# Optimization experiments

Measured on AMD Instinct MI355X. Metric: run time of the kernel, lower is better.

## Reference

```python
import jax, jax.numpy as jnp
import numpy as np
from jax import lax

B, T, H = 2, 1024, 2048
NH, D = 8, 128          # heads, head_dim
P = NH * D              # projection size
K = 4                   # short conv kernel size
EPS = 1e-6
SCALE = D ** -0.5


def _causal_conv_silu(x, w):
    # x: (B,T,C); w: (C,K) depthwise causal conv followed by silu (ShortConvolution)
    C = w.shape[0]
    kern = jnp.transpose(w)[:, None, :]  # (K,1,C)
    y = lax.conv_general_dilated(x, kern, window_strides=(1,), padding=[(K - 1, 0)],
                                 dimension_numbers=('NWC', 'WIO', 'NWC'),
                                 feature_group_count=C)
    return jax.nn.silu(y)


def _l2norm(x):
    return x * jax.lax.rsqrt(jnp.sum(x * x, axis=-1, keepdims=True) + EPS)


def _forward(hidden_states, Wq, Wk, Wv, conv_q, conv_k, conv_v, A_log, dt_bias,
             Wfa, Wfb, Wb, Wga, Wgb, norm_weight, Wo):
    x = hidden_states                                # (B,T,H)
    q = _causal_conv_silu(x @ Wq.T, conv_q)          # (B,T,P)
    k = _causal_conv_silu(x @ Wk.T, conv_k)
    v = _causal_conv_silu(x @ Wv.T, conv_v)
    # fused_kda_gate: g = -exp(A_log) * softplus(f_b(f_a(x)) + dt_bias), per (h,d) channel
    gf = (x @ Wfa.T) @ Wfb.T                         # (B,T,P) low-rank gate proj
    gf = gf.reshape(B, T, NH, D) + dt_bias.reshape(NH, D)
    g = -jnp.exp(A_log)[None, None, :, None] * jax.nn.softplus(gf)  # (B,T,NH,D) log-decay <= 0
    beta = jax.nn.sigmoid(x @ Wb.T)                  # (B,T,NH)
    q = _l2norm(q.reshape(B, T, NH, D)) * SCALE      # use_qk_l2norm_in_kernel + 1/sqrt(d) scale
    k = _l2norm(k.reshape(B, T, NH, D))
    v = v.reshape(B, T, NH, D)

    # gated delta-rule recurrence (KDA): per-key-channel decay, beta-weighted delta update
    def step(S, inp):
        q_t, k_t, v_t, g_t, b_t = inp                # (B,NH,D), beta (B,NH)
        S = S * jnp.exp(g_t)[..., None]              # decay rows (key dim) of S[.,.,dk,dv]
        kv = jnp.einsum('bhk,bhkv->bhv', k_t, S)
        delta = (v_t - kv) * b_t[..., None]
        S = S + jnp.einsum('bhk,bhv->bhkv', k_t, delta)
        o_t = jnp.einsum('bhk,bhkv->bhv', q_t, S)
        return S, o_t

    tfirst = lambda a: jnp.moveaxis(a, 1, 0)         # time-major for scan
    S0 = jnp.zeros((B, NH, D, D), x.dtype)
    _, o = lax.scan(step, S0, (tfirst(q), tfirst(k), tfirst(v), tfirst(g), tfirst(beta)))
    o = jnp.moveaxis(o, 0, 1)                        # (B,T,NH,D)

    # FusedRMSNormGated(sigmoid): gate applied before RMS normalization (Mamba2 convention)
    gate = ((x @ Wga.T) @ Wgb.T).reshape(B, T, NH, D)
    og = o * jax.nn.sigmoid(gate)
    og = og * jax.lax.rsqrt(jnp.mean(og * og, axis=-1, keepdims=True) + EPS) * norm_weight
    return og.reshape(B * T, P) @ Wo.T               # (B*T, H)


def setup_inputs():
    ks = jax.random.split(jax.random.key(0), 16)
    s = 0.02
    f32 = jnp.float32
    return {
        'hidden_states': jax.random.normal(ks[0], (B, T, H), f32),
        'Wq': jax.random.normal(ks[1], (P, H), f32) * s,
        'Wk': jax.random.normal(ks[2], (P, H), f32) * s,
        'Wv': jax.random.normal(ks[3], (P, H), f32) * s,
        'conv_q': jax.random.normal(ks[4], (P, K), f32) * 0.3,
        'conv_k': jax.random.normal(ks[5], (P, K), f32) * 0.3,
        'conv_v': jax.random.normal(ks[6], (P, K), f32) * 0.3,
        'A_log': jnp.log(jax.random.uniform(ks[7], (NH,), f32, 1.0, 16.0)),
        'dt_bias': jax.random.normal(ks[8], (P,), f32) * 0.5,
        'Wfa': jax.random.normal(ks[9], (D, H), f32) * s,
        'Wfb': jax.random.normal(ks[10], (P, D), f32) * s,
        'Wb': jax.random.normal(ks[11], (NH, H), f32) * s,
        'Wga': jax.random.normal(ks[12], (D, H), f32) * s,
        'Wgb': jax.random.normal(ks[13], (P, D), f32) * s,
        'norm_weight': jnp.ones((D,), f32),
        'Wo': jax.random.normal(ks[14], (H, P), f32) * s,
    }


def reference(hidden_states, Wq, Wk, Wv, conv_q, conv_k, conv_v, A_log, dt_bias,
              Wfa, Wfb, Wb, Wga, Wgb, norm_weight, Wo):
    return _forward(hidden_states, Wq, Wk, Wv, conv_q, conv_k, conv_v, A_log, dt_bias,
                    Wfa, Wfb, Wb, Wga, Wgb, norm_weight, Wo)
```

## Files before the change

kernel.cpp:

```cpp
#include <hip/hip_runtime.h>
#include <hip/hip_bf16.h>
#include <cstddef>
#include <cstdint>

#define Bb 2
#define Tt 1024
#define Hh 2048
#define NHh 8
#define Dd 128
#define Pp (NHh * Dd)
#define Kk 4
#define EPSf 1e-6f
#define SCALEf 0.08838834764831845f
#define DVQ 16
#define CHUNK 8

typedef short bf16x8 __attribute__((ext_vector_type(8)));
typedef float f32x4 __attribute__((ext_vector_type(4)));
typedef float f32x2 __attribute__((ext_vector_type(2)));

template <int CTRL>
__device__ __forceinline__ float dpp_add(float x) {
  int yi = __builtin_amdgcn_update_dpp(0, __builtin_bit_cast(int, x), CTRL, 0xF, 0xF, true);
  return x + __builtin_bit_cast(float, yi);
}
__device__ __forceinline__ float row16_sum(float x) {
  x = dpp_add<0xB1>(x);
  x = dpp_add<0x4E>(x);
  x = dpp_add<0x124>(x);
  x = dpp_add<0x128>(x);
  return x;
}

__device__ __forceinline__ void gload_lds16(const void* g, void* l) {
  __builtin_amdgcn_global_load_lds((const __attribute__((address_space(1))) void*)g,
                                   (__attribute__((address_space(3))) void*)l, 16, 0, 0);
}

__global__ __launch_bounds__(256) void cvt_bf16(const float* __restrict__ src,
                                                __hip_bfloat16* __restrict__ dst, int n) {
  const int i = (blockIdx.x * 256 + threadIdx.x) * 8;
  if (i >= n) return;
  const float4 a = *reinterpret_cast<const float4*>(src + i);
  const float4 b = *reinterpret_cast<const float4*>(src + i + 4);
  __hip_bfloat16 t[8];
  t[0] = __float2bfloat16(a.x); t[1] = __float2bfloat16(a.y);
  t[2] = __float2bfloat16(a.z); t[3] = __float2bfloat16(a.w);
  t[4] = __float2bfloat16(b.x); t[5] = __float2bfloat16(b.y);
  t[6] = __float2bfloat16(b.z); t[7] = __float2bfloat16(b.w);
  *reinterpret_cast<uint4*>(dst + i) = *reinterpret_cast<const uint4*>(t);
}

__global__ __launch_bounds__(256) void cvt_bf16_x4(const float* __restrict__ s0,
                                                   const float* __restrict__ s1,
                                                   const float* __restrict__ s2,
                                                   const float* __restrict__ s3,
                                                   __hip_bfloat16* __restrict__ d0,
                                                   __hip_bfloat16* __restrict__ d1,
                                                   __hip_bfloat16* __restrict__ d2,
                                                   __hip_bfloat16* __restrict__ d3,
                                                   int nper) {
  const int bpa = nper / 2048;
  const int a = blockIdx.x / bpa;
  const int i = (blockIdx.x % bpa) * 2048 + threadIdx.x * 8;
  const float* src = (a == 0) ? s0 : (a == 1) ? s1 : (a == 2) ? s2 : s3;
  __hip_bfloat16* dst = (a == 0) ? d0 : (a == 1) ? d1 : (a == 2) ? d2 : d3;
  const float4 x = *reinterpret_cast<const float4*>(src + i);
  const float4 y = *reinterpret_cast<const float4*>(src + i + 4);
  __hip_bfloat16 t[8];
  t[0] = __float2bfloat16(x.x); t[1] = __float2bfloat16(x.y);
  t[2] = __float2bfloat16(x.z); t[3] = __float2bfloat16(x.w);
  t[4] = __float2bfloat16(y.x); t[5] = __float2bfloat16(y.y);
  t[6] = __float2bfloat16(y.z); t[7] = __float2bfloat16(y.w);
  *reinterpret_cast<uint4*>(dst + i) = *reinterpret_cast<const uint4*>(t);
}

__global__ __launch_bounds__(256) void cvt_split(const float* __restrict__ src,
                                                 __hip_bfloat16* __restrict__ hi,
                                                 __hip_bfloat16* __restrict__ lo, int n) {
  const int i = (blockIdx.x * 256 + threadIdx.x) * 8;
  if (i >= n) return;
  __hip_bfloat16 th[8], tl[8];
#pragma unroll
  for (int j = 0; j < 2; j++) {
    const float4 a = *reinterpret_cast<const float4*>(src + i + j * 4);
    const float f[4] = {a.x, a.y, a.z, a.w};
#pragma unroll
    for (int e = 0; e < 4; e++) {
      const __hip_bfloat16 h = __float2bfloat16(f[e]);
      th[j * 4 + e] = h;
      tl[j * 4 + e] = __float2bfloat16(f[e] - __bfloat162float(h));
    }
  }
  *reinterpret_cast<uint4*>(hi + i) = *reinterpret_cast<const uint4*>(th);
  *reinterpret_cast<uint4*>(lo + i) = *reinterpret_cast<const uint4*>(tl);
}

__global__ __launch_bounds__(256) void gemm_nn_split(const float* __restrict__ A,
                                                     const float* __restrict__ B,
                                                     __hip_bfloat16* __restrict__ Chi,
                                                     __hip_bfloat16* __restrict__ Clo,
                                                     int M, int N, int K, int mode) {
  __shared__ float As[64][33];
  __shared__ float Bs[32][65];
  const int bm = blockIdx.y * 64, bn = blockIdx.x * 64;
  const int tid = threadIdx.x;
  const int tx = tid & 15, ty = tid >> 4;
  float acc[4][4];
#pragma unroll
  for (int i = 0; i < 4; i++)
#pragma unroll
    for (int j = 0; j < 4; j++) acc[i][j] = 0.f;
  for (int k0 = 0; k0 < K; k0 += 32) {
#pragma unroll
    for (int i = 0; i < 8; i++) {
      const int idx = tid + i * 256;
      const int r = idx >> 5, c = idx & 31;
      As[r][c] = A[(size_t)(bm + r) * K + k0 + c];
    }
#pragma unroll
    for (int i = 0; i < 8; i++) {
      const int idx = tid + i * 256;
      const int r = idx >> 6, c = idx & 63;
      Bs[r][c] = B[(size_t)(k0 + r) * N + bn + c];
    }
    __syncthreads();
#pragma unroll
    for (int kk = 0; kk < 32; kk++) {
      float a[4], b[4];
#pragma unroll
      for (int i = 0; i < 4; i++) a[i] = As[ty * 4 + i][kk];
#pragma unroll
      for (int j = 0; j < 4; j++) b[j] = Bs[kk][tx * 4 + j];
#pragma unroll
      for (int i = 0; i < 4; i++)
#pragma unroll
        for (int j = 0; j < 4; j++) acc[i][j] += a[i] * b[j];
    }
    __syncthreads();
  }
#pragma unroll
  for (int i = 0; i < 4; i++) {
    const int row = bm + ty * 4 + i;
#pragma unroll
    for (int j = 0; j < 4; j++) {
      const int col = bn + tx * 4 + j;
      const float v = acc[i][j];
      const __hip_bfloat16 h = __float2bfloat16(v);
      Chi[(size_t)row * N + col] = h;
      if (mode == 0) Clo[(size_t)row * N + col] = __float2bfloat16(v - __bfloat162float(h));
    }
  }
}

__global__ __launch_bounds__(256) void gemm_bf16_lds(const __hip_bfloat16* __restrict__ A,
                                                     const __hip_bfloat16* __restrict__ B,
                                                     float* __restrict__ C,
                                                     __hip_bfloat16* __restrict__ Cbf,
                                                     int M, int N, int K, int outmode) {
  __shared__ __align__(16) __hip_bfloat16 As[128 * 64];
  __shared__ __align__(16) __hip_bfloat16 Bs[128 * 64];
  const int tid = threadIdx.x;
  const int wave = tid >> 6;
  const int lane = tid & 63;
  const int wm = (wave >> 1) * 64;
  const int wn = (wave & 1) * 64;
  const int bm = blockIdx.y * 128;
  const int bn = blockIdx.x * 128;
  const int l15 = lane & 15;
  const int l4 = lane >> 4;
  const int srow = lane >> 3;
  const int scol = (lane & 7) * 8;

  f32x4 acc[4][4];
#pragma unroll
  for (int i = 0; i < 4; i++)
#pragma unroll
    for (int j = 0; j < 4; j++) acc[i][j] = (f32x4){0.f, 0.f, 0.f, 0.f};

  for (int k0 = 0; k0 < K; k0 += 64) {
#pragma unroll
    for (int i = 0; i < 4; i++) {
      const int s = wave * 4 + i;
      const int row = s * 8 + srow;
      gload_lds16(A + (size_t)(bm + row) * K + k0 + scol, &As[s * 512]);
      gload_lds16(B + (size_t)(bn + row) * K + k0 + scol, &Bs[s * 512]);
    }
    __syncthreads();
    bf16x8 af[4][2], bfv[4][2];
#pragma unroll
    for (int kf = 0; kf < 2; kf++) {
      const int kc = kf * 32 + l4 * 8;
#pragma unroll
      for (int mf = 0; mf < 4; mf++)
        af[mf][kf] = *reinterpret_cast<const bf16x8*>(&As[(wm + mf * 16 + l15) * 64 + kc]);
#pragma unroll
      for (int nf = 0; nf < 4; nf++)
        bfv[nf][kf] = *reinterpret_cast<const bf16x8*>(&Bs[(wn + nf * 16 + l15) * 64 + kc]);
    }
#pragma unroll
    for (int kf = 0; kf < 2; kf++)
#pragma unroll
      for (int mf = 0; mf < 4; mf++)
#pragma unroll
        for (int nf = 0; nf < 4; nf++)
          acc[mf][nf] = __builtin_amdgcn_mfma_f32_16x16x32_bf16(af[mf][kf], bfv[nf][kf],
                                                                acc[mf][nf], 0, 0, 0);
    __syncthreads();
  }
#pragma unroll
  for (int mf = 0; mf < 4; mf++) {
#pragma unroll
    for (int nf = 0; nf < 4; nf++) {
      const int col = bn + wn + nf * 16 + l15;
#pragma unroll
      for (int r = 0; r < 4; r++) {
        const int row = bm + wm + mf * 16 + l4 * 4 + r;
        if (outmode == 0) C[(size_t)row * N + col] = acc[mf][nf][r];
        else Cbf[(size_t)row * N + col] = __float2bfloat16(acc[mf][nf][r]);
      }
    }
  }
}

__global__ __launch_bounds__(256) void gemm_bf16_3t_lds(const __hip_bfloat16* __restrict__ Ahi,
                                                        const __hip_bfloat16* __restrict__ Alo,
                                                        const __hip_bfloat16* __restrict__ Bhi,
                                                        const __hip_bfloat16* __restrict__ Blo,
                                                        float* __restrict__ C,
                                                        int M, int N, int K,
                                                        const float* __restrict__ dtb,
                                                        const float* __restrict__ A_log,
                                                        int gmode) {
  __shared__ __align__(16) __hip_bfloat16 Ahs[64 * 64];
  __shared__ __align__(16) __hip_bfloat16 Als[64 * 64];
  __shared__ __align__(16) __hip_bfloat16 Bhs[128 * 64];
  __shared__ __align__(16) __hip_bfloat16 Bls[128 * 64];
  const int tid = threadIdx.x;
  const int wave = tid >> 6;
  const int lane = tid & 63;
  const int wm = (wave >> 1) * 32;
  const int wn = (wave & 1) * 64;
  const int bm = blockIdx.y * 64;
  const int bn = blockIdx.x * 128;
  const int l15 = lane & 15;
  const int l4 = lane >> 4;
  const int srow = lane >> 3;
  const int scol = (lane & 7) * 8;

  f32x4 acc[2][4];
#pragma unroll
  for (int i = 0; i < 2; i++)
#pragma unroll
    for (int j = 0; j < 4; j++) acc[i][j] = (f32x4){0.f, 0.f, 0.f, 0.f};

  for (int k0 = 0; k0 < K; k0 += 64) {
#pragma unroll
    for (int i = 0; i < 12; i++) {
      const int sid = wave * 12 + i;
      if (sid < 8) {
        const int row = sid * 8 + srow;
        gload_lds16(Ahi + (size_t)(bm + row) * K + k0 + scol, &Ahs[sid * 512]);
      } else if (sid < 16) {
        const int row = (sid - 8) * 8 + srow;
        gload_lds16(Alo + (size_t)(bm + row) * K + k0 + scol, &Als[(sid - 8) * 512]);
      } else if (sid < 32) {
        const int row = (sid - 16) * 8 + srow;
        gload_lds16(Bhi + (size_t)(bn + row) * K + k0 + scol, &Bhs[(sid - 16) * 512]);
      } else {
        const int row = (sid - 32) * 8 + srow;
        gload_lds16(Blo + (size_t)(bn + row) * K + k0 + scol, &Bls[(sid - 32) * 512]);
      }
    }
    __syncthreads();
#pragma unroll
    for (int kf = 0; kf < 2; kf++) {
      const int kc = kf * 32 + l4 * 8;
      bf16x8 ah[2], al[2], bh[4], bl[4];
#pragma unroll
      for (int mf = 0; mf < 2; mf++) {
        ah[mf] = *reinterpret_cast<const bf16x8*>(&Ahs[(wm + mf * 16 + l15) * 64 + kc]);
        al[mf] = *reinterpret_cast<const bf16x8*>(&Als[(wm + mf * 16 + l15) * 64 + kc]);
      }
#pragma unroll
      for (int nf = 0; nf < 4; nf++) {
        bh[nf] = *reinterpret_cast<const bf16x8*>(&Bhs[(wn + nf * 16 + l15) * 64 + kc]);
        bl[nf] = *reinterpret_cast<const bf16x8*>(&Bls[(wn + nf * 16 + l15) * 64 + kc]);
      }
#pragma unroll
      for (int mf = 0; mf < 2; mf++)
#pragma unroll
        for (int nf = 0; nf < 4; nf++) {
          acc[mf][nf] = __builtin_amdgcn_mfma_f32_16x16x32_bf16(ah[mf], bh[nf], acc[mf][nf], 0, 0, 0);
          acc[mf][nf] = __builtin_amdgcn_mfma_f32_16x16x32_bf16(ah[mf], bl[nf], acc[mf][nf], 0, 0, 0);
          acc[mf][nf] = __builtin_amdgcn_mfma_f32_16x16x32_bf16(al[mf], bh[nf], acc[mf][nf], 0, 0, 0);
        }
    }
    __syncthreads();
  }
#pragma unroll
  for (int mf = 0; mf < 2; mf++)
#pragma unroll
    for (int nf = 0; nf < 4; nf++) {
      const int col = bn + wn + nf * 16 + l15;
#pragma unroll
      for (int r = 0; r < 4; r++) {
        const int row = bm + wm + mf * 16 + l4 * 4 + r;
        float val = acc[mf][nf][r];
        if (gmode) {
          const float xv = val + dtb[col];
          const float sp = (xv > 20.f) ? xv : log1pf(expf(xv));
          val = expf(-expf(A_log[col >> 7]) * sp);
        }
        C[(size_t)row * N + col] = val;
      }
    }
}

__global__ __launch_bounds__(256) void gemm_nt(const float* __restrict__ A,
                                               const float* __restrict__ Bm,
                                               float* __restrict__ C,
                                               int M, int N, int Kd) {
  __shared__ float As[16][64];
  __shared__ float Bs[16][64];
  const int bm = blockIdx.y * 64;
  const int bn = blockIdx.x * 64;
  const int tid = threadIdx.x;
  const int tx = tid & 15;
  const int ty = tid >> 4;
  const int lr = tid >> 2;
  const int lc = (tid & 3) << 2;
  float acc[4][4];
#pragma unroll
  for (int i = 0; i < 4; i++)
#pragma unroll
    for (int j = 0; j < 4; j++) acc[i][j] = 0.f;
  for (int k0 = 0; k0 < Kd; k0 += 16) {
    float4 a4 = make_float4(0.f, 0.f, 0.f, 0.f);
    float4 b4 = make_float4(0.f, 0.f, 0.f, 0.f);
    const int ar = bm + lr;
    if (ar < M) a4 = *reinterpret_cast<const float4*>(A + (size_t)ar * Kd + k0 + lc);
    const int br = bn + lr;
    if (br < N) b4 = *reinterpret_cast<const float4*>(Bm + (size_t)br * Kd + k0 + lc);
    As[lc + 0][lr] = a4.x; As[lc + 1][lr] = a4.y; As[lc + 2][lr] = a4.z; As[lc + 3][lr] = a4.w;
    Bs[lc + 0][lr] = b4.x; Bs[lc + 1][lr] = b4.y; Bs[lc + 2][lr] = b4.z; Bs[lc + 3][lr] = b4.w;
    __syncthreads();
#pragma unroll
    for (int kk = 0; kk < 16; kk++) {
      float4 av = *reinterpret_cast<const float4*>(&As[kk][ty << 2]);
      float4 bv = *reinterpret_cast<const float4*>(&Bs[kk][tx << 2]);
      float a[4] = {av.x, av.y, av.z, av.w};
      float b[4] = {bv.x, bv.y, bv.z, bv.w};
#pragma unroll
      for (int i = 0; i < 4; i++)
#pragma unroll
        for (int j = 0; j < 4; j++) acc[i][j] += a[i] * b[j];
    }
    __syncthreads();
  }
#pragma unroll
  for (int i = 0; i < 4; i++) {
    const int row = bm + (ty << 2) + i;
    if (row >= M) continue;
#pragma unroll
    for (int j = 0; j < 4; j++) {
      const int col = bn + (tx << 2) + j;
      if (col < N) C[(size_t)row * N + col] = acc[i][j];
    }
  }
}

__global__ __launch_bounds__(256) void beta_kernel(const float* __restrict__ x,
                                                   const float* __restrict__ Wb,
                                                   float* __restrict__ beta) {
  __shared__ float xs[Hh];
  const int m = blockIdx.x;
  const int tid = threadIdx.x;
  for (int i = tid; i < Hh; i += 256) xs[i] = x[(size_t)m * Hh + i];
  __syncthreads();
  const int h = tid >> 5;
  const int lane = tid & 31;
  float acc = 0.f;
  for (int i = lane; i < Hh; i += 32) acc += xs[i] * Wb[(size_t)h * Hh + i];
#pragma unroll
  for (int o = 16; o > 0; o >>= 1) acc += __shfl_down(acc, o, 32);
  if (lane == 0) beta[(size_t)m * NHh + h] = 1.f / (1.f + expf(-acc));
}

__global__ __launch_bounds__(256) void g_kernel(float* __restrict__ gbuf,
                                                const float* __restrict__ dtb,
                                                const float* __restrict__ A_log) {
  const size_t i = (size_t)blockIdx.x * 256 + threadIdx.x;
  const int c = (int)(i % Pp);
  const int h = c / Dd;
  const float xv = gbuf[i] + dtb[c];
  const float sp = (xv > 20.f) ? xv : log1pf(expf(xv));
  gbuf[i] = expf(-expf(A_log[h]) * sp);
}

__global__ __launch_bounds__(128) void conv_silu_norm(const float* __restrict__ xin,
                                                      const float* __restrict__ w,
                                                      float* __restrict__ out,
                                                      int mode, int instride, int coff) {
  const int idx = blockIdx.x;
  const int h = idx % NHh;
  const int bt = idx / NHh;
  const int t = bt % Tt;
  const int d = threadIdx.x;
  const int c = h * Dd + d;
  float acc = 0.f;
#pragma unroll
  for (int j = 0; j < Kk; j++) {
    const int tt = t - (Kk - 1) + j;
    float xv = 0.f;
    if (tt >= 0) xv = xin[(size_t)(bt - (Kk - 1) + j) * instride + coff + c];
    acc += w[c * Kk + j] * xv;
  }
  float y = acc / (1.f + expf(-acc));
  float r = y;
  if (mode > 0) {
    float ss = y * y;
#pragma unroll
    for (int o = 32; o > 0; o >>= 1) ss += __shfl_down(ss, o);
    __shared__ float red[2];
    if ((d & 63) == 0) red[d >> 6] = ss;
    __syncthreads();
    const float tot = red[0] + red[1];
    const float inv = rsqrtf(tot + EPSf);
    r = y * inv * (mode == 2 ? SCALEf : 1.f);
  }
  out[(size_t)bt * Pp + c] = r;
}

__global__ __launch_bounds__(128) void conv3b_kernel(const float* __restrict__ qkvpre,
                                                     const float* __restrict__ cq,
                                                     const float* __restrict__ ck,
                                                     const float* __restrict__ cv,
                                                     float* __restrict__ outbase) {
  const int nper = (Bb * Tt / 4) * NHh;
  const int which = blockIdx.x / nper;
  const int idx = blockIdx.x % nper;
  const float* w = (which == 0) ? cq : (which == 1) ? ck : cv;
  const int mode = (which == 0) ? 2 : (which == 1) ? 1 : 0;
  const int h = idx % NHh;
  const int bt0 = (idx / NHh) * 4;
  const int t0 = bt0 % Tt;
  const int d = threadIdx.x;
  const int c = h * Dd + d;

  float xw[7];
#pragma unroll
  for (int i = 0; i < 7; i++) {
    const int tt = t0 - 3 + i;
    xw[i] = (tt >= 0) ? qkvpre[(size_t)(bt0 - 3 + i) * (4 * Pp) + which * Pp + c] : 0.f;
  }
  const float w0 = w[c * Kk + 0], w1 = w[c * Kk + 1], w2 = w[c * Kk + 2], w3 = w[c * Kk + 3];
  float y[4];
#pragma unroll
  for (int jj = 0; jj < 4; jj++) {
    const float a = w0 * xw[jj] + w1 * xw[jj + 1] + w2 * xw[jj + 2] + w3 * xw[jj + 3];
    y[jj] = a / (1.f + expf(-a));
  }
  if (mode > 0) {
    float ss[4];
#pragma unroll
    for (int jj = 0; jj < 4; jj++) ss[jj] = y[jj] * y[jj];
#pragma unroll
    for (int o = 32; o > 0; o >>= 1) {
#pragma unroll
      for (int jj = 0; jj < 4; jj++) ss[jj] += __shfl_down(ss[jj], o);
    }
    __shared__ float red[2][4];
    if ((d & 63) == 0) {
#pragma unroll
      for (int jj = 0; jj < 4; jj++) red[d >> 6][jj] = ss[jj];
    }
    __syncthreads();
    const float sc = (mode == 2) ? SCALEf : 1.f;
#pragma unroll
    for (int jj = 0; jj < 4; jj++)
      y[jj] = y[jj] * rsqrtf(red[0][jj] + red[1][jj] + EPSf) * sc;
  }
  float* outp = outbase + (size_t)which * (Bb * Tt) * Pp;
#pragma unroll
  for (int jj = 0; jj < 4; jj++) outp[(size_t)(bt0 + jj) * Pp + c] = y[jj];
}

__global__ __launch_bounds__(128) void scan_kernel(const float* __restrict__ q,
                                                   const float* __restrict__ k,
                                                   const float* __restrict__ v,
                                                   const float* __restrict__ eg,
                                                   const float* __restrict__ beta,
                                                   float* __restrict__ o) {
  const int blk = blockIdx.x;
  const int bh = blk & 15;
  const int dvq = blk >> 4;
  const int b = bh >> 3, h = bh & 7;
  const int tid = threadIdx.x;
  const int qr = tid & 15;
  const int dvl = tid >> 4;
  const int dv = dvq * 8 + dvl;

  __shared__ __align__(16) float qs[2][CHUNK][16][12];
  __shared__ __align__(16) float ks[2][CHUNK][16][12];
  __shared__ __align__(16) float legs[2][CHUNK][16][12];
  __shared__ float vs[2][CHUNK][8];
  __shared__ float betas[2][CHUNK];

  f32x2 s2[4];
#pragma unroll
  for (int i = 0; i < 4; i++) s2[i] = (f32x2){0.f, 0.f};

  const size_t base = (size_t)(b * Tt) * Pp + h * Dd;
  const int le = tid;

  float rq[CHUNK], rk[CHUNK], re[CHUNK], rv[CHUNK], rb = 0.f;
  auto load_chunk = [&](int t0) {
    const size_t coff = base + (size_t)t0 * Pp;
#pragma unroll
    for (int j = 0; j < CHUNK; j++) {
      rq[j] = q[coff + (size_t)j * Pp + le];
      rk[j] = k[coff + (size_t)j * Pp + le];
      re[j] = eg[coff + (size_t)j * Pp + le];
    }
    if (tid < 8) {
#pragma unroll
      for (int j = 0; j < CHUNK; j++) rv[j] = v[coff + (size_t)j * Pp + dvq * 8 + tid];
    } else if (tid < 8 + CHUNK) {
      rb = beta[(size_t)(b * Tt + t0 + tid - 8) * NHh + h];
    }
  };
  auto write_lds = [&](int bufw) {
#pragma unroll
    for (int j = 0; j < CHUNK; j++) {
      qs[bufw][j][le >> 3][le & 7] = rq[j];
      ks[bufw][j][le >> 3][le & 7] = rk[j];
      legs[bufw][j][le >> 3][le & 7] = re[j];
    }
    if (tid < 8) {
#pragma unroll
      for (int j = 0; j < CHUNK; j++) vs[bufw][j][tid] = rv[j];
    } else if (tid < 8 + CHUNK) {
      betas[bufw][tid - 8] = rb;
    }
  };
  auto unpack = [](const float4& a, const float4& b, f32x2 out[4]) {
    out[0] = (f32x2){a.x, a.y}; out[1] = (f32x2){a.z, a.w};
    out[2] = (f32x2){b.x, b.y}; out[3] = (f32x2){b.z, b.w};
  };

  load_chunk(0);
  write_lds(0);
  __syncthreads();
  const int NC = Tt / CHUNK;
  size_t off = base;
  for (int c = 0; c < NC; c++) {
    if (c + 1 < NC) load_chunk((c + 1) * CHUNK);
    const int buf = c & 1;
    float vv[CHUNK], bb[CHUNK], opart[CHUNK];
#pragma unroll
    for (int j = 0; j < CHUNK; j++) { vv[j] = vs[buf][j][dvl]; bb[j] = betas[buf][j]; }

    f32x2 ck2[4], ce2[4], cq2[4], kt2[4];
    {
      const float4 k0 = *reinterpret_cast<const float4*>(&ks[buf][0][qr][0]);
      const float4 k1 = *reinterpret_cast<const float4*>(&ks[buf][0][qr][4]);
      const float4 e0 = *reinterpret_cast<const float4*>(&legs[buf][0][qr][0]);
      const float4 e1 = *reinterpret_cast<const float4*>(&legs[buf][0][qr][4]);
      const float4 q0 = *reinterpret_cast<const float4*>(&qs[buf][0][qr][0]);
      const float4 q1 = *reinterpret_cast<const float4*>(&qs[buf][0][qr][4]);
      unpack(k0, k1, ck2); unpack(e0, e1, ce2); unpack(q0, q1, cq2);
#pragma unroll
      for (int i = 0; i < 4; i++) kt2[i] = ck2[i] * ce2[i];
    }

#pragma unroll
    for (int j = 0; j < CHUNK; j++) {
      float4 nk0, nk1, ne0, ne1, nq0, nq1;
      if (j + 1 < CHUNK) {
        nk0 = *reinterpret_cast<const float4*>(&ks[buf][j + 1][qr][0]);
        nk1 = *reinterpret_cast<const float4*>(&ks[buf][j + 1][qr][4]);
        ne0 = *reinterpret_cast<const float4*>(&legs[buf][j + 1][qr][0]);
        ne1 = *reinterpret_cast<const float4*>(&legs[buf][j + 1][qr][4]);
        nq0 = *reinterpret_cast<const float4*>(&qs[buf][j + 1][qr][0]);
        nq1 = *reinterpret_cast<const float4*>(&qs[buf][j + 1][qr][4]);
      }
      f32x2 es0 = ce2[0] * s2[0], es1 = ce2[1] * s2[1];
      f32x2 es2v = ce2[2] * s2[2], es3 = ce2[3] * s2[3];
      f32x2 kva = kt2[0] * s2[0];
      f32x2 kvb = kt2[1] * s2[1];
      kva = kt2[2] * s2[2] + kva;
      kvb = kt2[3] * s2[3] + kvb;
      kva = kva + kvb;
      const float kvp = row16_sum(kva.x + kva.y);
      const float delta = (vv[j] - kvp) * bb[j];
      const f32x2 d2 = (f32x2){delta, delta};
      f32x2 o2;
      s2[0] = ck2[0] * d2 + es0;  o2 = cq2[0] * s2[0];
      s2[1] = ck2[1] * d2 + es1;  o2 = cq2[1] * s2[1] + o2;
      s2[2] = ck2[2] * d2 + es2v; o2 = cq2[2] * s2[2] + o2;
      s2[3] = ck2[3] * d2 + es3;  o2 = cq2[3] * s2[3] + o2;
      opart[j] = o2.x + o2.y;
      if (j + 1 < CHUNK) {
        unpack(nk0, nk1, ck2); unpack(ne0, ne1, ce2); unpack(nq0, nq1, cq2);
#pragma unroll
        for (int i = 0; i < 4; i++) kt2[i] = ck2[i] * ce2[i];
      }
    }
#pragma unroll
    for (int j = 0; j < CHUNK; j++) opart[j] = row16_sum(opart[j]);
    if (qr == 0) {
#pragma unroll
      for (int j = 0; j < CHUNK; j++) o[off + (size_t)j * Pp + dv] = opart[j];
    }
    if (c + 1 < NC) write_lds(buf ^ 1);
    __syncthreads();
    off += (size_t)CHUNK * Pp;
  }
}

__global__ __launch_bounds__(128) void gated_norm(float* __restrict__ o,
                                                  const float* __restrict__ gate,
                                                  int gstride,
                                                  const float* __restrict__ nw,
                                                  __hip_bfloat16* __restrict__ ogbf) {
  const int idx = blockIdx.x;
  const int h = idx % NHh;
  const int bt = idx / NHh;
  const int d = threadIdx.x;
  const size_t off = (size_t)bt * Pp + h * Dd;
  const float ov = o[off + d];
  const float gt = gate[(size_t)bt * gstride + h * Dd + d];
  const float val = ov / (1.f + expf(-gt));
  float ss = val * val;
#pragma unroll
  for (int sh = 32; sh > 0; sh >>= 1) ss += __shfl_down(ss, sh);
  __shared__ float red[2];
  if ((d & 63) == 0) red[d >> 6] = ss;
  __syncthreads();
  const float mean = (red[0] + red[1]) * (1.f / Dd);
  const float res = val * rsqrtf(mean + EPSf) * nw[d];
  if (ogbf != nullptr) ogbf[off + d] = __float2bfloat16(res);
  else o[off + d] = res;
}

extern "C" void kernel_launch(void* const* d_in, const int* in_sizes, int n_in,
                              void* d_out, int out_size, void* d_ws, size_t ws_size,
                              hipStream_t stream) {
  const float* x     = (const float*)d_in[0];
  const float* Wq    = (const float*)d_in[1];
  const float* Wk    = (const float*)d_in[2];
  const float* Wv    = (const float*)d_in[3];
  const float* cq    = (const float*)d_in[4];
  const float* ck    = (const float*)d_in[5];
  const float* cv    = (const float*)d_in[6];
  const float* A_log = (const float*)d_in[7];
  const float* dtb   = (const float*)d_in[8];
  const float* Wfa   = (const float*)d_in[9];
  const float* Wfb   = (const float*)d_in[10];
  const float* Wb    = (const float*)d_in[11];
  const float* Wga   = (const float*)d_in[12];
  const float* Wgb   = (const float*)d_in[13];
  const float* nw    = (const float*)d_in[14];
  const float* Wo    = (const float*)d_in[15];
  float* outp = (float*)d_out;

  const int M = Bb * Tt;
  const size_t MP = (size_t)M * Pp;
  float* ws = (float*)d_ws;
  float* qkvpre = ws;
  float* qb   = qkvpre + 4 * MP;
  float* kb   = qb + MP;
  float* vb   = kb + MP;
  float* gbuf = vb + MP;
  float* obuf = gbuf + MP;
  float* betab = obuf + MP;
  float* gfa  = betab + (size_t)M * NHh;
  float* gga  = gfa + (size_t)M * Dd;
  float* f32end = gga + (size_t)M * Dd;

  __hip_bfloat16* xhi    = (__hip_bfloat16*)f32end;
  __hip_bfloat16* xlo    = xhi + (size_t)M * Hh;
  __hip_bfloat16* Wqkvbf = xlo + (size_t)M * Hh;
  __hip_bfloat16* Wobf   = Wqkvbf + (size_t)4 * Pp * Hh;
  __hip_bfloat16* Wcombhi = Wobf + (size_t)Hh * Pp;
  __hip_bfloat16* Wcomblo = Wcombhi + (size_t)Pp * Hh;
  __hip_bfloat16* end = Wcomblo + (size_t)Pp * Hh;
  __hip_bfloat16* ogbf = xlo;
  const bool use_mfma = ws_size >= (size_t)((char*)end - (char*)d_ws);

  const dim3 blk(256);
  if (use_mfma) {
    cvt_split<<<(int)((size_t)M * Hh / 2048), blk, 0, stream>>>(x, xhi, xlo, M * Hh);
    cvt_bf16_x4<<<4 * (int)((size_t)Pp * Hh / 2048), blk, 0, stream>>>(
        Wq, Wk, Wv, Wo, Wqkvbf, Wqkvbf + (size_t)Pp * Hh, Wqkvbf + (size_t)2 * Pp * Hh,
        Wobf, Pp * Hh);
    gemm_nn_split<<<dim3(Hh / 64, Pp / 64), blk, 0, stream>>>(Wfb, Wfa, Wcombhi, Wcomblo,
                                                              Pp, Hh, Dd, 0);
    gemm_nn_split<<<dim3(Hh / 64, Pp / 64), blk, 0, stream>>>(Wgb, Wga,
                                                              Wqkvbf + (size_t)3 * Pp * Hh,
                                                              nullptr, Pp, Hh, Dd, 1);
    gemm_bf16_lds<<<dim3(4 * Pp / 128, M / 128), blk, 0, stream>>>(xhi, Wqkvbf, qkvpre, nullptr,
                                                                   M, 4 * Pp, Hh, 0);
    gemm_bf16_3t_lds<<<dim3(Pp / 128, M / 64), blk, 0, stream>>>(xhi, xlo, Wcombhi, Wcomblo,
                                                                 gbuf, M, Pp, Hh,
                                                                 dtb, A_log, 1);
    beta_kernel<<<M, 256, 0, stream>>>(x, Wb, betab);
    conv3b_kernel<<<3 * (M / 4) * NHh, 128, 0, stream>>>(qkvpre, cq, ck, cv, qb);
    scan_kernel<<<Bb * NHh * DVQ, 128, 0, stream>>>(qb, kb, vb, gbuf, betab, obuf);
    gated_norm<<<M * NHh, 128, 0, stream>>>(obuf, qkvpre + (size_t)3 * Pp, 4 * Pp, nw, ogbf);
    gemm_bf16_lds<<<dim3(Hh / 128, M / 128), blk, 0, stream>>>(ogbf, Wobf, outp, nullptr,
                                                               M, Hh, Pp, 0);
  } else {
    float* qpre = qkvpre;
    float* kpre = qkvpre + MP;
    float* vpre = qkvpre + 2 * MP;
    float* gate = qkvpre + 3 * MP;
    gemm_nt<<<dim3(Pp / 64, M / 64), blk, 0, stream>>>(x, Wq, qpre, M, Pp, Hh);
    gemm_nt<<<dim3(Pp / 64, M / 64), blk, 0, stream>>>(x, Wk, kpre, M, Pp, Hh);
    gemm_nt<<<dim3(Pp / 64, M / 64), blk, 0, stream>>>(x, Wv, vpre, M, Pp, Hh);
    gemm_nt<<<dim3(Dd / 64, M / 64), blk, 0, stream>>>(x, Wfa, gfa, M, Dd, Hh);
    gemm_nt<<<dim3(Dd / 64, M / 64), blk, 0, stream>>>(x, Wga, gga, M, Dd, Hh);
    gemm_nt<<<dim3(Pp / 64, M / 64), blk, 0, stream>>>(gfa, Wfb, gbuf, M, Pp, Dd);
    gemm_nt<<<dim3(Pp / 64, M / 64), blk, 0, stream>>>(gga, Wgb, gate, M, Pp, Dd);
    beta_kernel<<<M, 256, 0, stream>>>(x, Wb, betab);
    g_kernel<<<(int)(MP / 256), 256, 0, stream>>>(gbuf, dtb, A_log);
    conv_silu_norm<<<M * NHh, 128, 0, stream>>>(qpre, cq, qb, 2, Pp, 0);
    conv_silu_norm<<<M * NHh, 128, 0, stream>>>(kpre, ck, kb, 1, Pp, 0);
    conv_silu_norm<<<M * NHh, 128, 0, stream>>>(vpre, cv, vb, 0, Pp, 0);
    scan_kernel<<<Bb * NHh * DVQ, 128, 0, stream>>>(qb, kb, vb, gbuf, betab, obuf);
    gated_norm<<<M * NHh, 128, 0, stream>>>(obuf, gate, Pp, nw, nullptr);
    gemm_nt<<<dim3(Hh / 64, M / 64), blk, 0, stream>>>(obuf, Wo, outp, M, Hh, Pp);
  }
}
```

Before: 446.4 us.

## Split scan into single-wave blocks over finer value slices and drop barriers

Result: slower. 540.7 us (+21.1%).

```diff
diff --git a/kernel.cpp b/kernel.cpp
--- a/kernel.cpp
+++ b/kernel.cpp
@@ -12,7 +12,7 @@
 #define Kk 4
 #define EPSf 1e-6f
 #define SCALEf 0.08838834764831845f
-#define DVQ 16
+#define DVQ32 32
 #define CHUNK 8
 
 typedef short bf16x8 __attribute__((ext_vector_type(8)));
@@ -486,25 +486,25 @@
   for (int jj = 0; jj < 4; jj++) outp[(size_t)(bt0 + jj) * Pp + c] = y[jj];
 }
 
-__global__ __launch_bounds__(128) void scan_kernel(const float* __restrict__ q,
-                                                   const float* __restrict__ k,
-                                                   const float* __restrict__ v,
-                                                   const float* __restrict__ eg,
-                                                   const float* __restrict__ beta,
-                                                   float* __restrict__ o) {
+__global__ __launch_bounds__(64) void scan_kernel(const float* __restrict__ q,
+                                                  const float* __restrict__ k,
+                                                  const float* __restrict__ v,
+                                                  const float* __restrict__ eg,
+                                                  const float* __restrict__ beta,
+                                                  float* __restrict__ o) {
   const int blk = blockIdx.x;
   const int bh = blk & 15;
   const int dvq = blk >> 4;
   const int b = bh >> 3, h = bh & 7;
-  const int tid = threadIdx.x;
-  const int qr = tid & 15;
-  const int dvl = tid >> 4;
-  const int dv = dvq * 8 + dvl;
+  const int lane = threadIdx.x;
+  const int qr = lane & 15;
+  const int dvl = lane >> 4;
+  const int dv = dvq * 4 + dvl;
 
   __shared__ __align__(16) float qs[2][CHUNK][16][12];
   __shared__ __align__(16) float ks[2][CHUNK][16][12];
   __shared__ __align__(16) float legs[2][CHUNK][16][12];
-  __shared__ float vs[2][CHUNK][8];
+  __shared__ float vs[2][CHUNK][4];
   __shared__ float betas[2][CHUNK];
 
   f32x2 s2[4];
@@ -512,36 +512,38 @@
   for (int i = 0; i < 4; i++) s2[i] = (f32x2){0.f, 0.f};
 
   const size_t base = (size_t)(b * Tt) * Pp + h * Dd;
-  const int le = tid;
-
-  float rq[CHUNK], rk[CHUNK], re[CHUNK], rv[CHUNK], rb = 0.f;
+
+  float rq[16], rk[16], re[16], rv = 0.f, rb = 0.f;
   auto load_chunk = [&](int t0) {
     const size_t coff = base + (size_t)t0 * Pp;
 #pragma unroll
-    for (int j = 0; j < CHUNK; j++) {
-      rq[j] = q[coff + (size_t)j * Pp + le];
-      rk[j] = k[coff + (size_t)j * Pp + le];
-      re[j] = eg[coff + (size_t)j * Pp + le];
-    }
-    if (tid < 8) {
-#pragma unroll
-      for (int j = 0; j < CHUNK; j++) rv[j] = v[coff + (size_t)j * Pp + dvq * 8 + tid];
-    } else if (tid < 8 + CHUNK) {
-      rb = beta[(size_t)(b * Tt + t0 + tid - 8) * NHh + h];
+    for (int r = 0; r < 16; r++) {
+      const int idx = lane + r * 64;
+      const int c = idx >> 7, ch = idx & 127;
+      const size_t g = coff + (size_t)c * Pp + ch;
+      rq[r] = q[g];
+      rk[r] = k[g];
+      re[r] = eg[g];
+    }
+    if (lane < 32) {
+      rv = v[coff + (size_t)(lane >> 2) * Pp + dvq * 4 + (lane & 3)];
+    } else if (lane < 32 + CHUNK) {
+      rb = beta[(size_t)(b * Tt + t0 + lane - 32) * NHh + h];
     }
   };
   auto write_lds = [&](int bufw) {
 #pragma unroll
-    for (int j = 0; j < CHUNK; j++) {
-      qs[bufw][j][le >> 3][le & 7] = rq[j];
-      ks[bufw][j][le >> 3][le & 7] = rk[j];
-      legs[bufw][j][le >> 3][le & 7] = re[j];
-    }
-    if (tid < 8) {
-#pragma unroll
-      for (int j = 0; j < CHUNK; j++) vs[bufw][j][tid] = rv[j];
-    } else if (tid < 8 + CHUNK) {
-      betas[bufw][tid - 8] = rb;
+    for (int r = 0; r < 16; r++) {
+      const int idx = lane + r * 64;
+      const int c = idx >> 7, ch = idx & 127;
+      qs[bufw][c][ch >> 3][ch & 7] = rq[r];
+      ks[bufw][c][ch >> 3][ch & 7] = rk[r];
+      legs[bufw][c][ch >> 3][ch & 7] = re[r];
+    }
+    if (lane < 32) {
+      vs[bufw][lane >> 2][lane & 3] = rv;
+    } else if (lane < 32 + CHUNK) {
+      betas[bufw][lane - 32] = rb;
     }
   };
   auto unpack = [](const float4& a, const float4& b, f32x2 out[4]) {
@@ -551,7 +553,6 @@
 
   load_chunk(0);
   write_lds(0);
-  __syncthreads();
   const int NC = Tt / CHUNK;
   size_t off = base;
   for (int c = 0; c < NC; c++) {
@@ -614,7 +615,6 @@
       for (int j = 0; j < CHUNK; j++) o[off + (size_t)j * Pp + dv] = opart[j];
     }
     if (c + 1 < NC) write_lds(buf ^ 1);
-    __syncthreads();
     off += (size_t)CHUNK * Pp;
   }
 }
@@ -707,7 +707,7 @@
                                                                  dtb, A_log, 1);
     beta_kernel<<<M, 256, 0, stream>>>(x, Wb, betab);
     conv3b_kernel<<<3 * (M / 4) * NHh, 128, 0, stream>>>(qkvpre, cq, ck, cv, qb);
-    scan_kernel<<<Bb * NHh * DVQ, 128, 0, stream>>>(qb, kb, vb, gbuf, betab, obuf);
+    scan_kernel<<<Bb * NHh * DVQ32, 64, 0, stream>>>(qb, kb, vb, gbuf, betab, obuf);
     gated_norm<<<M * NHh, 128, 0, stream>>>(obuf, qkvpre + (size_t)3 * Pp, 4 * Pp, nw, ogbf);
     gemm_bf16_lds<<<dim3(Hh / 128, M / 128), blk, 0, stream>>>(ogbf, Wobf, outp, nullptr,
                                                                M, Hh, Pp, 0);
@@ -728,7 +728,7 @@
     conv_silu_norm<<<M * NHh, 128, 0, stream>>>(qpre, cq, qb, 2, Pp, 0);
     conv_silu_norm<<<M * NHh, 128, 0, stream>>>(kpre, ck, kb, 1, Pp, 0);
     conv_silu_norm<<<M * NHh, 128, 0, stream>>>(vpre, cv, vb, 0, Pp, 0);
-    scan_kernel<<<Bb * NHh * DVQ, 128, 0, stream>>>(qb, kb, vb, gbuf, betab, obuf);
+    scan_kernel<<<Bb * NHh * DVQ32, 64, 0, stream>>>(qb, kb, vb, gbuf, betab, obuf);
     gated_norm<<<M * NHh, 128, 0, stream>>>(obuf, gate, Pp, nw, nullptr);
     gemm_nt<<<dim3(Hh / 64, M / 64), blk, 0, stream>>>(obuf, Wo, outp, M, Hh, Pp);
   }
```

## Drop split-bf16 gate GEMM and fold gate projection into fused QKV GEMM

Applied to the files above, without the earlier changes.

Result: faster. 411.6 us, median of 2 (-7.8%).

```diff
diff --git a/kernel.cpp b/kernel.cpp
--- a/kernel.cpp
+++ b/kernel.cpp
@@ -9,6 +9,7 @@
 #define NHh 8
 #define Dd 128
 #define Pp (NHh * Dd)
+#define NW (5 * Pp)
 #define Kk 4
 #define EPSf 1e-6f
 #define SCALEf 0.08838834764831845f
@@ -75,32 +76,10 @@
   *reinterpret_cast<uint4*>(dst + i) = *reinterpret_cast<const uint4*>(t);
 }
 
-__global__ __launch_bounds__(256) void cvt_split(const float* __restrict__ src,
-                                                 __hip_bfloat16* __restrict__ hi,
-                                                 __hip_bfloat16* __restrict__ lo, int n) {
-  const int i = (blockIdx.x * 256 + threadIdx.x) * 8;
-  if (i >= n) return;
-  __hip_bfloat16 th[8], tl[8];
-#pragma unroll
-  for (int j = 0; j < 2; j++) {
-    const float4 a = *reinterpret_cast<const float4*>(src + i + j * 4);
-    const float f[4] = {a.x, a.y, a.z, a.w};
-#pragma unroll
-    for (int e = 0; e < 4; e++) {
-      const __hip_bfloat16 h = __float2bfloat16(f[e]);
-      th[j * 4 + e] = h;
-      tl[j * 4 + e] = __float2bfloat16(f[e] - __bfloat162float(h));
-    }
-  }
-  *reinterpret_cast<uint4*>(hi + i) = *reinterpret_cast<const uint4*>(th);
-  *reinterpret_cast<uint4*>(lo + i) = *reinterpret_cast<const uint4*>(tl);
-}
-
-__global__ __launch_bounds__(256) void gemm_nn_split(const float* __restrict__ A,
-                                                     const float* __restrict__ B,
-                                                     __hip_bfloat16* __restrict__ Chi,
-                                                     __hip_bfloat16* __restrict__ Clo,
-                                                     int M, int N, int K, int mode) {
+__global__ __launch_bounds__(256) void gemm_nn_bf16(const float* __restrict__ A,
+                                                    const float* __restrict__ B,
+                                                    __hip_bfloat16* __restrict__ Cbf,
+                                                    int M, int N, int K) {
   __shared__ float As[64][33];
   __shared__ float Bs[32][65];
   const int bm = blockIdx.y * 64, bn = blockIdx.x * 64;
@@ -145,10 +124,7 @@
 #pragma unroll
     for (int j = 0; j < 4; j++) {
       const int col = bn + tx * 4 + j;
-      const float v = acc[i][j];
-      const __hip_bfloat16 h = __float2bfloat16(v);
-      Chi[(size_t)row * N + col] = h;
-      if (mode == 0) Clo[(size_t)row * N + col] = __float2bfloat16(v - __bfloat162float(h));
+      Cbf[(size_t)row * N + col] = __float2bfloat16(acc[i][j]);
     }
   }
 }
@@ -223,100 +199,6 @@
   }
 }
 
-__global__ __launch_bounds__(256) void gemm_bf16_3t_lds(const __hip_bfloat16* __restrict__ Ahi,
-                                                        const __hip_bfloat16* __restrict__ Alo,
-                                                        const __hip_bfloat16* __restrict__ Bhi,
-                                                        const __hip_bfloat16* __restrict__ Blo,
-                                                        float* __restrict__ C,
-                                                        int M, int N, int K,
-                                                        const float* __restrict__ dtb,
-                                                        const float* __restrict__ A_log,
-                                                        int gmode) {
-  __shared__ __align__(16) __hip_bfloat16 Ahs[64 * 64];
-  __shared__ __align__(16) __hip_bfloat16 Als[64 * 64];
-  __shared__ __align__(16) __hip_bfloat16 Bhs[128 * 64];
-  __shared__ __align__(16) __hip_bfloat16 Bls[128 * 64];
-  const int tid = threadIdx.x;
-  const int wave = tid >> 6;
-  const int lane = tid & 63;
-  const int wm = (wave >> 1) * 32;
-  const int wn = (wave & 1) * 64;
-  const int bm = blockIdx.y * 64;
-  const int bn = blockIdx.x * 128;
-  const int l15 = lane & 15;
-  const int l4 = lane >> 4;
-  const int srow = lane >> 3;
-  const int scol = (lane & 7) * 8;
-
-  f32x4 acc[2][4];
-#pragma unroll
-  for (int i = 0; i < 2; i++)
-#pragma unroll
-    for (int j = 0; j < 4; j++) acc[i][j] = (f32x4){0.f, 0.f, 0.f, 0.f};
-
-  for (int k0 = 0; k0 < K; k0 += 64) {
-#pragma unroll
-    for (int i = 0; i < 12; i++) {
-      const int sid = wave * 12 + i;
-      if (sid < 8) {
-        const int row = sid * 8 + srow;
-        gload_lds16(Ahi + (size_t)(bm + row) * K + k0 + scol, &Ahs[sid * 512]);
-      } else if (sid < 16) {
-        const int row = (sid - 8) * 8 + srow;
-        gload_lds16(Alo + (size_t)(bm + row) * K + k0 + scol, &Als[(sid - 8) * 512]);
-      } else if (sid < 32) {
-        const int row = (sid - 16) * 8 + srow;
-        gload_lds16(Bhi + (size_t)(bn + row) * K + k0 + scol, &Bhs[(sid - 16) * 512]);
-      } else {
-        const int row = (sid - 32) * 8 + srow;
-        gload_lds16(Blo + (size_t)(bn + row) * K + k0 + scol, &Bls[(sid - 32) * 512]);
-      }
-    }
-    __syncthreads();
-#pragma unroll
-    for (int kf = 0; kf < 2; kf++) {
-      const int kc = kf * 32 + l4 * 8;
-      bf16x8 ah[2], al[2], bh[4], bl[4];
-#pragma unroll
-      for (int mf = 0; mf < 2; mf++) {
-        ah[mf] = *reinterpret_cast<const bf16x8*>(&Ahs[(wm + mf * 16 + l15) * 64 + kc]);
-        al[mf] = *reinterpret_cast<const bf16x8*>(&Als[(wm + mf * 16 + l15) * 64 + kc]);
-      }
-#pragma unroll
-      for (int nf = 0; nf < 4; nf++) {
-        bh[nf] = *reinterpret_cast<const bf16x8*>(&Bhs[(wn + nf * 16 + l15) * 64 + kc]);
-        bl[nf] = *reinterpret_cast<const bf16x8*>(&Bls[(wn + nf * 16 + l15) * 64 + kc]);
-      }
-#pragma unroll
-      for (int mf = 0; mf < 2; mf++)
-#pragma unroll
-        for (int nf = 0; nf < 4; nf++) {
-          acc[mf][nf] = __builtin_amdgcn_mfma_f32_16x16x32_bf16(ah[mf], bh[nf], acc[mf][nf], 0, 0, 0);
-          acc[mf][nf] = __builtin_amdgcn_mfma_f32_16x16x32_bf16(ah[mf], bl[nf], acc[mf][nf], 0, 0, 0);
-          acc[mf][nf] = __builtin_amdgcn_mfma_f32_16x16x32_bf16(al[mf], bh[nf], acc[mf][nf], 0, 0, 0);
-        }
-    }
-    __syncthreads();
-  }
-#pragma unroll
-  for (int mf = 0; mf < 2; mf++)
-#pragma unroll
-    for (int nf = 0; nf < 4; nf++) {
-      const int col = bn + wn + nf * 16 + l15;
-#pragma unroll
-      for (int r = 0; r < 4; r++) {
-        const int row = bm + wm + mf * 16 + l4 * 4 + r;
-        float val = acc[mf][nf][r];
-        if (gmode) {
-          const float xv = val + dtb[col];
-          const float sp = (xv > 20.f) ? xv : log1pf(expf(xv));
-          val = expf(-expf(A_log[col >> 7]) * sp);
-        }
-        C[(size_t)row * N + col] = val;
-      }
-    }
-}
-
 __global__ __launch_bounds__(256) void gemm_nt(const float* __restrict__ A,
                                                const float* __restrict__ Bm,
                                                float* __restrict__ C,
@@ -387,15 +269,18 @@
   if (lane == 0) beta[(size_t)m * NHh + h] = 1.f / (1.f + expf(-acc));
 }
 
-__global__ __launch_bounds__(256) void g_kernel(float* __restrict__ gbuf,
+__global__ __launch_bounds__(256) void g_kernel(const float* __restrict__ src,
+                                                int sstride, int scol,
+                                                float* __restrict__ dst,
                                                 const float* __restrict__ dtb,
                                                 const float* __restrict__ A_log) {
   const size_t i = (size_t)blockIdx.x * 256 + threadIdx.x;
   const int c = (int)(i % Pp);
+  const size_t row = i / Pp;
   const int h = c / Dd;
-  const float xv = gbuf[i] + dtb[c];
+  const float xv = src[row * sstride + scol + c] + dtb[c];
   const float sp = (xv > 20.f) ? xv : log1pf(expf(xv));
-  gbuf[i] = expf(-expf(A_log[h]) * sp);
+  dst[i] = expf(-expf(A_log[h]) * sp);
 }
 
 __global__ __launch_bounds__(128) void conv_silu_norm(const float* __restrict__ xin,
@@ -436,7 +321,8 @@
                                                      const float* __restrict__ cq,
                                                      const float* __restrict__ ck,
                                                      const float* __restrict__ cv,
-                                                     float* __restrict__ outbase) {
+                                                     float* __restrict__ outbase,
+                                                     int instride) {
   const int nper = (Bb * Tt / 4) * NHh;
   const int which = blockIdx.x / nper;
   const int idx = blockIdx.x % nper;
@@ -452,7 +338,7 @@
 #pragma unroll
   for (int i = 0; i < 7; i++) {
     const int tt = t0 - 3 + i;
-    xw[i] = (tt >= 0) ? qkvpre[(size_t)(bt0 - 3 + i) * (4 * Pp) + which * Pp + c] : 0.f;
+    xw[i] = (tt >= 0) ? qkvpre[(size_t)(bt0 - 3 + i) * instride + which * Pp + c] : 0.f;
   }
   const float w0 = w[c * Kk + 0], w1 = w[c * Kk + 1], w2 = w[c * Kk + 2], w3 = w[c * Kk + 3];
   float y[4];
@@ -669,7 +555,7 @@
   const size_t MP = (size_t)M * Pp;
   float* ws = (float*)d_ws;
   float* qkvpre = ws;
-  float* qb   = qkvpre + 4 * MP;
+  float* qb   = qkvpre + (size_t)M * NW;
   float* kb   = qb + MP;
   float* vb   = kb + MP;
   float* gbuf = vb + MP;
@@ -680,35 +566,31 @@
   float* f32end = gga + (size_t)M * Dd;
 
   __hip_bfloat16* xhi    = (__hip_bfloat16*)f32end;
-  __hip_bfloat16* xlo    = xhi + (size_t)M * Hh;
-  __hip_bfloat16* Wqkvbf = xlo + (size_t)M * Hh;
-  __hip_bfloat16* Wobf   = Wqkvbf + (size_t)4 * Pp * Hh;
-  __hip_bfloat16* Wcombhi = Wobf + (size_t)Hh * Pp;
-  __hip_bfloat16* Wcomblo = Wcombhi + (size_t)Pp * Hh;
-  __hip_bfloat16* end = Wcomblo + (size_t)Pp * Hh;
-  __hip_bfloat16* ogbf = xlo;
+  __hip_bfloat16* Wqkvbf = xhi + (size_t)M * Hh;
+  __hip_bfloat16* Wobf   = Wqkvbf + (size_t)NW * Hh;
+  __hip_bfloat16* end    = Wobf + (size_t)Hh * Pp;
+  __hip_bfloat16* ogbf   = (__hip_bfloat16*)qb;
   const bool use_mfma = ws_size >= (size_t)((char*)end - (char*)d_ws);
 
   const dim3 blk(256);
   if (use_mfma) {
-    cvt_split<<<(int)((size_t)M * Hh / 2048), blk, 0, stream>>>(x, xhi, xlo, M * Hh);
+    cvt_bf16<<<(int)((size_t)M * Hh / 2048), blk, 0, stream>>>(x, xhi, M * Hh);
     cvt_bf16_x4<<<4 * (int)((size_t)Pp * Hh / 2048), blk, 0, stream>>>(
         Wq, Wk, Wv, Wo, Wqkvbf, Wqkvbf + (size_t)Pp * Hh, Wqkvbf + (size_t)2 * Pp * Hh,
         Wobf, Pp * Hh);
-    gemm_nn_split<<<dim3(Hh / 64, Pp / 64), blk, 0, stream>>>(Wfb, Wfa, Wcombhi, Wcomblo,
-                                                              Pp, Hh, Dd, 0);
-    gemm_nn_split<<<dim3(Hh / 64, Pp / 64), blk, 0, stream>>>(Wgb, Wga,
-                                                              Wqkvbf + (size_t)3 * Pp * Hh,
-                                                              nullptr, Pp, Hh, Dd, 1);
-    gemm_bf16_lds<<<dim3(4 * Pp / 128, M / 128), blk, 0, stream>>>(xhi, Wqkvbf, qkvpre, nullptr,
-                                                                   M, 4 * Pp, Hh, 0);
-    gemm_bf16_3t_lds<<<dim3(Pp / 128, M / 64), blk, 0, stream>>>(xhi, xlo, Wcombhi, Wcomblo,
-                                                                 gbuf, M, Pp, Hh,
-                                                                 dtb, A_log, 1);
+    gemm_nn_bf16<<<dim3(Hh / 64, Pp / 64), blk, 0, stream>>>(Wgb, Wga,
+                                                             Wqkvbf + (size_t)3 * Pp * Hh,
+                                                             Pp, Hh, Dd);
+    gemm_nn_bf16<<<dim3(Hh / 64, Pp / 64), blk, 0, stream>>>(Wfb, Wfa,
+                                                             Wqkvbf + (size_t)4 * Pp * Hh,
+                                                             Pp, Hh, Dd);
+    gemm_bf16_lds<<<dim3(NW / 128, M / 128), blk, 0, stream>>>(xhi, Wqkvbf, qkvpre, nullptr,
+                                                               M, NW, Hh, 0);
+    g_kernel<<<(int)(MP / 256), blk, 0, stream>>>(qkvpre, NW, 4 * Pp, gbuf, dtb, A_log);
     beta_kernel<<<M, 256, 0, stream>>>(x, Wb, betab);
-    conv3b_kernel<<<3 * (M / 4) * NHh, 128, 0, stream>>>(qkvpre, cq, ck, cv, qb);
+    conv3b_kernel<<<3 * (M / 4) * NHh, 128, 0, stream>>>(qkvpre, cq, ck, cv, qb, NW);
     scan_kernel<<<Bb * NHh * DVQ, 128, 0, stream>>>(qb, kb, vb, gbuf, betab, obuf);
-    gated_norm<<<M * NHh, 128, 0, stream>>>(obuf, qkvpre + (size_t)3 * Pp, 4 * Pp, nw, ogbf);
+    gated_norm<<<M * NHh, 128, 0, stream>>>(obuf, qkvpre + (size_t)3 * Pp, NW, nw, ogbf);
     gemm_bf16_lds<<<dim3(Hh / 128, M / 128), blk, 0, stream>>>(ogbf, Wobf, outp, nullptr,
                                                                M, Hh, Pp, 0);
   } else {
@@ -724,7 +606,7 @@
     gemm_nt<<<dim3(Pp / 64, M / 64), blk, 0, stream>>>(gfa, Wfb, gbuf, M, Pp, Dd);
     gemm_nt<<<dim3(Pp / 64, M / 64), blk, 0, stream>>>(gga, Wgb, gate, M, Pp, Dd);
     beta_kernel<<<M, 256, 0, stream>>>(x, Wb, betab);
-    g_kernel<<<(int)(MP / 256), 256, 0, stream>>>(gbuf, dtb, A_log);
+    g_kernel<<<(int)(MP / 256), blk, 0, stream>>>(gbuf, Pp, 0, gbuf, dtb, A_log);
     conv_silu_norm<<<M * NHh, 128, 0, stream>>>(qpre, cq, qb, 2, Pp, 0);
     conv_silu_norm<<<M * NHh, 128, 0, stream>>>(kpre, ck, kb, 1, Pp, 0);
     conv_silu_norm<<<M * NHh, 128, 0, stream>>>(vpre, cv, vb, 0, Pp, 0);
```
